# Performance work log

Measured on AMD Instinct MI355X. Metric: run time of the kernel, lower is better.

The kernel has to match this reference:

```python
import jax, jax.numpy as jnp
import numpy as np

NEG = -1e9  # stand-in for -inf mask fill (avoids NaN, softmax weight ~0)
EPS = 1e-5  # torch LayerNorm default


def layer_norm(x, g, b):
    mu = jnp.mean(x, axis=-1, keepdims=True)
    var = jnp.mean(jnp.square(x - mu), axis=-1, keepdims=True)
    return (x - mu) * jax.lax.rsqrt(var + EPS) * g + b


def _forward(x, context, batch_lengths, max_len,
             Wq1, Wk1, Wv1, Wq2, Wk2, Wv2,
             ln1_g, ln1_b, ln2_g, ln2_b, ln3_g, ln3_b,
             fc1_w, fc1_b, fc2_w, fc2_b):
    B, L, E = x.shape
    H, _, dk = Wq1.shape
    pos = jnp.arange(L)
    valid = pos[None, :] < batch_lengths[:, None]                  # [B,L]
    out_mask = valid[:, :, None].astype(x.dtype)                   # [B,L,1] (outputMask)
    key_bias = jnp.where(valid, 0.0, NEG)[:, None, None, :]        # [B,1,1,L] (attnMask on keys)
    causal_bias = jnp.where(pos[:, None] >= pos[None, :], 0.0, NEG)  # [L,L] decoding mask
    scale = 1.0 / jnp.sqrt(jnp.asarray(dk, x.dtype))

    def mha(qk_src, v_src, Wq, Wk, Wv, causal):
        # Q,K from qk_src, V from v_src (faithful to Head.forward)
        m = out_mask[:, None]                                      # [B,1,L,1]
        Q = jnp.einsum('ble,hed->bhld', qk_src, Wq) * m
        K = jnp.einsum('ble,hed->bhld', qk_src, Wk) * m
        V = jnp.einsum('ble,hed->bhld', v_src, Wv) * m
        e = jnp.einsum('bhid,bhjd->bhij', Q, K) + key_bias
        if causal:
            e = e + causal_bias
        s = jax.nn.softmax(e * scale, axis=-1)
        o = jnp.einsum('bhij,bhjd->bhid', s, V)
        return o.transpose(0, 2, 1, 3).reshape(B, L, E)            # concat heads

    z = mha(x, x, Wq1, Wk1, Wv1, causal=True) * out_mask
    x1 = layer_norm(x + z, ln1_g, ln1_b)
    # cross block: Q,K from context, V from x1 (as in source)
    z = mha(context, x1, Wq2, Wk2, Wv2, causal=False) * out_mask
    x2 = layer_norm(x1 + z, ln2_g, ln2_b)
    h = jax.nn.relu(x2 @ fc1_w + fc1_b) * out_mask
    z = (h @ fc2_w + fc2_b) * out_mask
    return layer_norm(x2 + z, ln3_g, ln3_b)


def setup_inputs() -> dict:
    B, L, E, H = 8, 1024, 1024, 16
    dk = E // H
    key = jax.random.key(0)
    ks = jax.random.split(key, 16)
    w = lambda k, s: jax.random.normal(k, s, jnp.float32) * 0.02
    return {
        'x': jax.random.normal(ks[0], (B, L, E), jnp.float32),
        'context': jax.random.normal(ks[1], (B, L, E), jnp.float32),
        'batch_lengths': jax.random.randint(ks[2], (B,), 1, L + 1),
        'max_len': L,
        'Wq1': w(ks[3], (H, E, dk)), 'Wk1': w(ks[4], (H, E, dk)), 'Wv1': w(ks[5], (H, E, dk)),
        'Wq2': w(ks[6], (H, E, dk)), 'Wk2': w(ks[7], (H, E, dk)), 'Wv2': w(ks[8], (H, E, dk)),
        'ln1_g': jnp.ones((E,), jnp.float32), 'ln1_b': jnp.zeros((E,), jnp.float32),
        'ln2_g': jnp.ones((E,), jnp.float32), 'ln2_b': jnp.zeros((E,), jnp.float32),
        'ln3_g': jnp.ones((E,), jnp.float32), 'ln3_b': jnp.zeros((E,), jnp.float32),
        'fc1_w': w(ks[9], (E, E)), 'fc1_b': jnp.zeros((E,), jnp.float32),
        'fc2_w': w(ks[10], (E, E)), 'fc2_b': jnp.zeros((E,), jnp.float32),
    }


def reference(x, context, batch_lengths, max_len,
              Wq1, Wk1, Wv1, Wq2, Wk2, Wv2,
              ln1_g, ln1_b, ln2_g, ln2_b, ln3_g, ln3_b,
              fc1_w, fc1_b, fc2_w, fc2_b):
    return _forward(x, context, batch_lengths, max_len,
                    Wq1, Wk1, Wv1, Wq2, Wk2, Wv2,
                    ln1_g, ln1_b, ln2_g, ln2_b, ln3_g, ln3_b,
                    fc1_w, fc1_b, fc2_w, fc2_b)
```

## Files before the change

### kernel.cpp

```cpp
#include <hip/hip_runtime.h>


typedef unsigned short u16;
typedef unsigned int u32;
typedef __attribute__((ext_vector_type(8))) short bf16x8;
typedef __attribute__((ext_vector_type(4))) float f32x4;

#define Bv 8
#define Lv 1024
#define Ev 1024
#define Hv 16
#define DKv 64
#define Mv (Bv * Lv)

#if defined(__has_builtin)
# if __has_builtin(__builtin_amdgcn_global_load_lds)
#  define HAS_GLL 1
# endif
#endif
#ifndef HAS_GLL
# define HAS_GLL 0
#endif

#if HAS_GLL
__device__ __forceinline__ void gll16(const u16* g, u16* l) {
    __builtin_amdgcn_global_load_lds(
        (const __attribute__((address_space(1))) void*)(unsigned long long)(g),
        (__attribute__((address_space(3))) void*)(unsigned)(unsigned long long)(l),
        16, 0, 0);
}
#endif

__device__ __forceinline__ u16 f2bf(float f) {
    u32 u = __float_as_uint(f);
    u += 0x7fffu + ((u >> 16) & 1u);
    return (u16)(u >> 16);
}
__device__ __forceinline__ u32 pack2(float a, float b) {
    u32 ua = __float_as_uint(a); ua += 0x7fffu + ((ua >> 16) & 1u);
    u32 ub = __float_as_uint(b); ub += 0x7fffu + ((ub >> 16) & 1u);
    return (ua >> 16) | (ub & 0xffff0000u);
}
__device__ __forceinline__ float bf_lo(u32 u) { return __uint_as_float(u << 16); }
__device__ __forceinline__ float bf_hi(u32 u) { return __uint_as_float(u & 0xffff0000u); }

__global__ __launch_bounds__(256) void prep_k(
    const float* __restrict__ x, const float* __restrict__ ctx,
    const float* __restrict__ wq1, const float* __restrict__ wk1, const float* __restrict__ wv1,
    const float* __restrict__ wq2, const float* __restrict__ wk2, const float* __restrict__ wv2,
    const float* __restrict__ f1, const float* __restrict__ f2,
    u16* __restrict__ xb, u16* __restrict__ cb, u16* __restrict__ WT) {
    const int id = blockIdx.x, t = threadIdx.x;
    if (id < 16384) {
        const float* s = (id < 8192) ? x : ctx;
        u16* d = (id < 8192) ? xb : cb;
        const int i4 = ((id & 8191) * 256 + t) * 4;
        float4 v = *(const float4*)(s + i4);
        uint2 o = {pack2(v.x, v.y), pack2(v.z, v.w)};
        *(uint2*)(d + i4) = o;
        return;
    }
    __shared__ float tl[32][33];
    const int tx = t & 31, ty = t >> 5;
    if (id < 16384 + 6144) {
        const int wi = (id - 16384) >> 10;
        const int tile = (id - 16384) & 1023;
        const float* s = (wi == 0) ? wq1 : (wi == 1) ? wk1 : (wi == 2) ? wv1
                       : (wi == 3) ? wq2 : (wi == 4) ? wk2 : wv2;
        u16* d = WT + (size_t)wi * Ev * Ev;
        const int h = tile >> 6, rem = tile & 63;
        const int d0 = (rem & 1) * 32, e0 = (rem >> 1) * 32;
#pragma unroll
        for (int i = 0; i < 4; i++)
            tl[ty + i * 8][tx] = s[(size_t)h * Ev * DKv + (size_t)(e0 + ty + i * 8) * DKv + d0 + tx];
        __syncthreads();
#pragma unroll
        for (int i = 0; i < 4; i++)
            d[(size_t)(h * DKv + d0 + ty + i * 8) * Ev + e0 + tx] = f2bf(tl[tx][ty + i * 8]);
    } else {
        const int wi = (id - 16384 - 6144) >> 10;
        const int tile = (id - 16384 - 6144) & 1023;
        const float* s = wi ? f2 : f1;
        u16* d = WT + (size_t)(6 + wi) * Ev * Ev;
        const int n0 = (tile & 31) * 32, k0 = (tile >> 5) * 32;
#pragma unroll
        for (int i = 0; i < 4; i++)
            tl[ty + i * 8][tx] = s[(size_t)(k0 + ty + i * 8) * Ev + n0 + tx];
        __syncthreads();
#pragma unroll
        for (int i = 0; i < 4; i++)
            d[(size_t)(n0 + ty + i * 8) * Ev + k0 + tx] = f2bf(tl[tx][ty + i * 8]);
    }
}

template <int BIAS, int RELU, int TRANSW>
__global__ __launch_bounds__(256) void mgemm(const u16* __restrict__ A,
                                             const u16* __restrict__ Wt,
                                             const float* __restrict__ bias,
                                             u16* __restrict__ O0, u16* __restrict__ O1,
                                             u16* __restrict__ O2,
                                             const int* __restrict__ lens) {
    __shared__ u16 Alds[2][16 * 512];
    __shared__ u16 Blds[2][16 * 512];
    const int tid = threadIdx.x;
    const int w = tid >> 6, l = tid & 63;
    const int lc = l & 15, lq = l >> 4;
    const int row0 = blockIdx.y * 128, col0 = blockIdx.x * 128;
    const int which = col0 >> 10, colL = col0 & 1023;
    u16* C = (which == 0) ? O0 : (which == 1 ? O1 : O2);
    const bool tr = (TRANSW == which);

    int len = lens[row0 >> 10];
    len = min(max(len, 0), Lv);
    if ((row0 & (Lv - 1)) >= len) {
        const int rr = tid >> 1, cc = (tid & 1) * 64;
        u16* p = tr ? C + (size_t)(colL + rr) * Mv + row0 + cc
                    : C + (size_t)(row0 + rr) * Ev + colL + cc;
        uint4 z4 = {0u, 0u, 0u, 0u};
#pragma unroll
        for (int i = 0; i < 8; i++) *(uint4*)(p + i * 8) = z4;
        return;
    }

    const int wm4 = (w >> 1) * 4, wn4 = (w & 1) * 4;
    f32x4 acc[4][4];
#pragma unroll
    for (int i = 0; i < 4; i++)
#pragma unroll
        for (int j = 0; j < 4; j++) acc[i][j] = (f32x4){0.f, 0.f, 0.f, 0.f};

    const u16* Ag[4]; const u16* Bg[4];
    int lof[4];
#pragma unroll
    for (int i = 0; i < 4; i++) {
        const int g16 = 2 * w + (i >> 1), k32 = i & 1;
        Ag[i] = A  + (size_t)(row0 + g16 * 16 + lc) * Ev + k32 * 32 + lq * 8;
        Bg[i] = Wt + (size_t)(col0 + g16 * 16 + lc) * Ev + k32 * 32 + lq * 8;
        lof[i] = (g16 * 2 + k32) * 512;
    }

#if HAS_GLL
#pragma unroll
    for (int i = 0; i < 4; i++) { gll16(Ag[i], &Alds[0][lof[i]]); gll16(Bg[i], &Blds[0][lof[i]]); }
#else
#pragma unroll
    for (int i = 0; i < 4; i++) {
        *(uint4*)(&Alds[0][lof[i] + l * 8]) = *(const uint4*)Ag[i];
        *(uint4*)(&Blds[0][lof[i] + l * 8]) = *(const uint4*)Bg[i];
    }
#endif
    __syncthreads();

    int cur = 0;
    for (int k0 = 0; k0 < Ev; k0 += 64) {
        if (k0 + 64 < Ev) {
            const int koff = k0 + 64;
#if HAS_GLL
#pragma unroll
            for (int i = 0; i < 4; i++) {
                gll16(Ag[i] + koff, &Alds[cur ^ 1][lof[i]]);
                gll16(Bg[i] + koff, &Blds[cur ^ 1][lof[i]]);
            }
#else
#pragma unroll
            for (int i = 0; i < 4; i++) {
                *(uint4*)(&Alds[cur ^ 1][lof[i] + l * 8]) = *(const uint4*)(Ag[i] + koff);
                *(uint4*)(&Blds[cur ^ 1][lof[i] + l * 8]) = *(const uint4*)(Bg[i] + koff);
            }
#endif
        }
        const u16* Ab = &Alds[cur][0];
        const u16* Bb = &Blds[cur][0];
#pragma unroll
        for (int km = 0; km < 2; km++) {
            bf16x8 af[4], bfr[4];
#pragma unroll
            for (int mt = 0; mt < 4; mt++)
                af[mt] = *(const bf16x8*)(Ab + ((wm4 + mt) * 2 + km) * 512 + l * 8);
#pragma unroll
            for (int nt = 0; nt < 4; nt++)
                bfr[nt] = *(const bf16x8*)(Bb + ((wn4 + nt) * 2 + km) * 512 + l * 8);
#pragma unroll
            for (int mt = 0; mt < 4; mt++)
#pragma unroll
                for (int nt = 0; nt < 4; nt++)
                    acc[mt][nt] = __builtin_amdgcn_mfma_f32_16x16x32_bf16(
                        af[mt], bfr[nt], acc[mt][nt], 0, 0, 0);
        }
        __syncthreads();
        cur ^= 1;
    }

    float bv[4];
#pragma unroll
    for (int nt = 0; nt < 4; nt++)
        bv[nt] = BIAS ? bias[colL + wn4 * 16 + nt * 16 + lc] : 0.f;

#pragma unroll
    for (int mt = 0; mt < 4; mt++) {
        const int rowb = row0 + wm4 * 16 + mt * 16 + lq * 4;
#pragma unroll
        for (int nt = 0; nt < 4; nt++) {
            const int col = colL + wn4 * 16 + nt * 16 + lc;
            float v[4];
#pragma unroll
            for (int r = 0; r < 4; r++) {
                float xv = acc[mt][nt][r] + bv[nt];
                if (RELU) xv = fmaxf(xv, 0.f);
                v[r] = (((rowb + r) & (Lv - 1)) >= len) ? 0.f : xv;
            }
            if (tr) {
                uint2 o = {pack2(v[0], v[1]), pack2(v[2], v[3])};
                *(uint2*)(C + (size_t)col * Mv + rowb) = o;
            } else {
#pragma unroll
                for (int r = 0; r < 4; r++)
                    C[(size_t)(rowb + r) * Ev + col] = f2bf(v[r]);
            }
        }
    }
}

template <int CAUSAL>
__global__ __launch_bounds__(256) void mattn(u16* __restrict__ QZ,
                                             const u16* __restrict__ K,
                                             const u16* __restrict__ VT,
                                             const int* __restrict__ lens) {
    __shared__ u16 Kt[2][16 * 512];
    __shared__ u16 Vt[2][16 * 512];
    __shared__ u16 Pt[4 * 4 * 512];
    const int b = blockIdx.z, h = blockIdx.y, qb = blockIdx.x;
    const int q0 = qb * 128;
    const int tid = threadIdx.x;
    const int w = tid >> 6, l = tid & 63;
    const int lc = l & 15, lq = l >> 4;
    int len = lens[b];
    len = min(max(len, 0), Lv);

    if (q0 >= len) {
        const int zr = tid >> 1, zc = (tid & 1) * 32;
        uint4 z4 = {0u, 0u, 0u, 0u};
        uint4* p = (uint4*)(QZ + (size_t)(b * Lv + q0 + zr) * Ev + h * DKv + zc);
        p[0] = z4; p[1] = z4; p[2] = z4; p[3] = z4;
        return;
    }

    bf16x8 qf[2][2];
#pragma unroll
    for (int mt = 0; mt < 2; mt++)
#pragma unroll
        for (int k2 = 0; k2 < 2; k2++)
            qf[mt][k2] = *(const bf16x8*)(QZ + (size_t)(b * Lv + q0 + w * 32 + mt * 16 + lc) * Ev +
                                          h * DKv + k2 * 32 + lq * 8);

    f32x4 of[2][4];
#pragma unroll
    for (int mt = 0; mt < 2; mt++)
#pragma unroll
        for (int nd = 0; nd < 4; nd++) of[mt][nd] = (f32x4){0.f, 0.f, 0.f, 0.f};
    float mrow[2][4], lrow[2][4];
#pragma unroll
    for (int mt = 0; mt < 2; mt++)
#pragma unroll
        for (int r = 0; r < 4; r++) { mrow[mt][r] = -1e30f; lrow[mt][r] = 0.f; }

    const u16* Kg[4]; const u16* Vg[4];
    int kof[4], vof[4];
#pragma unroll
    for (int i = 0; i < 4; i++) {
        const int k16 = 2 * w + (i >> 1), d32 = i & 1;
        Kg[i] = K + (size_t)(b * Lv + k16 * 16 + lc) * Ev + h * DKv + d32 * 32 + lq * 8;
        kof[i] = (k16 * 2 + d32) * 512;
        Vg[i] = VT + (size_t)(h * DKv + w * 16 + lc) * Mv + b * Lv + i * 32 + lq * 8;
        vof[i] = (w * 4 + i) * 512;
    }
    u16* Pw = Pt + w * 2048;

    const int jend = CAUSAL ? min(len, q0 + 128) : len;
    const int ntiles = (jend + 127) >> 7;

#if HAS_GLL
#pragma unroll
    for (int i = 0; i < 4; i++) {
        gll16(Kg[i], &Kt[0][kof[i]]);
        gll16(Vg[i], &Vt[0][vof[i]]);
    }
#else
#pragma unroll
    for (int i = 0; i < 4; i++) {
        *(uint4*)(&Kt[0][kof[i] + l * 8]) = *(const uint4*)Kg[i];
        *(uint4*)(&Vt[0][vof[i] + l * 8]) = *(const uint4*)Vg[i];
    }
#endif
    __syncthreads();

    int cur = 0;
    for (int kt = 0; kt < ntiles; kt++) {
        const int koff = kt * 128;
        if (kt + 1 < ntiles) {
            const int knext = koff + 128;
#if HAS_GLL
#pragma unroll
            for (int i = 0; i < 4; i++) {
                gll16(Kg[i] + (size_t)knext * Ev, &Kt[cur ^ 1][kof[i]]);
                gll16(Vg[i] + knext, &Vt[cur ^ 1][vof[i]]);
            }
#else
#pragma unroll
            for (int i = 0; i < 4; i++) {
                *(uint4*)(&Kt[cur ^ 1][kof[i] + l * 8]) = *(const uint4*)(Kg[i] + (size_t)knext * Ev);
                *(uint4*)(&Vt[cur ^ 1][vof[i] + l * 8]) = *(const uint4*)(Vg[i] + knext);
            }
#endif
        }
        const u16* Kb = &Kt[cur][0];
        const u16* Vb = &Vt[cur][0];

        f32x4 sf[2][8];
#pragma unroll
        for (int nt = 0; nt < 8; nt++) {
            bf16x8 kf0 = *(const bf16x8*)(Kb + (nt * 2 + 0) * 512 + l * 8);
            bf16x8 kf1 = *(const bf16x8*)(Kb + (nt * 2 + 1) * 512 + l * 8);
#pragma unroll
            for (int mt = 0; mt < 2; mt++) {
                f32x4 s = (f32x4){0.f, 0.f, 0.f, 0.f};
                s = __builtin_amdgcn_mfma_f32_16x16x32_bf16(qf[mt][0], kf0, s, 0, 0, 0);
                s = __builtin_amdgcn_mfma_f32_16x16x32_bf16(qf[mt][1], kf1, s, 0, 0, 0);
                sf[mt][nt] = s;
            }
        }

        float alpha[2][4];
#pragma unroll
        for (int mt = 0; mt < 2; mt++) {
            float tmax[4] = {-1e30f, -1e30f, -1e30f, -1e30f};
#pragma unroll
            for (int nt = 0; nt < 8; nt++) {
                const int jj = koff + nt * 16 + lc;
                const bool jv = jj < len;
#pragma unroll
                for (int r = 0; r < 4; r++) {
                    const int iq = q0 + w * 32 + mt * 16 + lq * 4 + r;
                    const bool valid = jv && (!CAUSAL || jj <= iq);
                    float e = valid ? sf[mt][nt][r] * 0.125f : -1e30f;
                    sf[mt][nt][r] = e;
                    tmax[r] = fmaxf(tmax[r], e);
                }
            }
#pragma unroll
            for (int r = 0; r < 4; r++) {
#pragma unroll
                for (int d = 1; d < 16; d <<= 1)
                    tmax[r] = fmaxf(tmax[r], __shfl_xor(tmax[r], d, 64));
            }
            float psum[4];
#pragma unroll
            for (int r = 0; r < 4; r++) {
                const float mn = fmaxf(mrow[mt][r], tmax[r]);
                alpha[mt][r] = __expf(mrow[mt][r] - mn);
                mrow[mt][r] = mn;
                psum[r] = 0.f;
            }
#pragma unroll
            for (int nt = 0; nt < 8; nt++)
#pragma unroll
                for (int r = 0; r < 4; r++) {
                    float p = __expf(sf[mt][nt][r] - mrow[mt][r]);
                    sf[mt][nt][r] = p;
                    psum[r] += p;
                }
#pragma unroll
            for (int r = 0; r < 4; r++) {
#pragma unroll
                for (int d = 1; d < 16; d <<= 1) psum[r] += __shfl_xor(psum[r], d, 64);
                lrow[mt][r] = lrow[mt][r] * alpha[mt][r] + psum[r];
            }
#pragma unroll
            for (int nd = 0; nd < 4; nd++)
#pragma unroll
                for (int r = 0; r < 4; r++) of[mt][nd][r] *= alpha[mt][r];
        }

#pragma unroll
        for (int mt = 0; mt < 2; mt++) {
#pragma unroll
            for (int nt = 0; nt < 8; nt++)
#pragma unroll
                for (int r = 0; r < 4; r++)
                    Pw[(nt >> 1) * 512 +
                       ((2 * (nt & 1) + (lc >> 3)) * 16 + lq * 4 + r) * 8 + (lc & 7)] =
                        f2bf(sf[mt][nt][r]);
#pragma unroll
            for (int km = 0; km < 4; km++) {
                bf16x8 pa = *(const bf16x8*)(Pw + km * 512 + l * 8);
#pragma unroll
                for (int nd = 0; nd < 4; nd++) {
                    bf16x8 vb = *(const bf16x8*)(Vb + (nd * 4 + km) * 512 + l * 8);
                    of[mt][nd] = __builtin_amdgcn_mfma_f32_16x16x32_bf16(pa, vb, of[mt][nd], 0, 0, 0);
                }
            }
        }
        __syncthreads();
        cur ^= 1;
    }

#pragma unroll
    for (int mt = 0; mt < 2; mt++) {
        float inv[4];
#pragma unroll
        for (int r = 0; r < 4; r++) {
            const int iq = q0 + w * 32 + mt * 16 + lq * 4 + r;
            inv[r] = (iq < len && lrow[mt][r] > 0.f) ? (1.f / lrow[mt][r]) : 0.f;
        }
#pragma unroll
        for (int nd = 0; nd < 4; nd++)
#pragma unroll
            for (int r = 0; r < 4; r++)
                QZ[(size_t)(b * Lv + q0 + w * 32 + mt * 16 + lq * 4 + r) * Ev +
                   h * DKv + nd * 16 + lc] = f2bf(of[mt][nd][r] * inv[r]);
    }
}

template <int BASEBF, int OUTF32>
__global__ __launch_bounds__(256) void ln_k(const void* __restrict__ base,
                                            const u16* __restrict__ z,
                                            const float* __restrict__ g,
                                            const float* __restrict__ bta,
                                            void* __restrict__ out) {
    __shared__ float w1[4], w2[4];
    const int row = blockIdx.x, t = threadIdx.x;
    const int w = t >> 6, l = t & 63;
    const int c0 = t * 4;
    float v[4];
    if (BASEBF) {
        uint2 bu = *(const uint2*)((const u16*)base + (size_t)row * Ev + c0);
        v[0] = bf_lo(bu.x); v[1] = bf_hi(bu.x); v[2] = bf_lo(bu.y); v[3] = bf_hi(bu.y);
    } else {
        float4 f = *(const float4*)((const float*)base + (size_t)row * Ev + c0);
        v[0] = f.x; v[1] = f.y; v[2] = f.z; v[3] = f.w;
    }
    uint2 zu = *(const uint2*)(z + (size_t)row * Ev + c0);
    v[0] += bf_lo(zu.x); v[1] += bf_hi(zu.x); v[2] += bf_lo(zu.y); v[3] += bf_hi(zu.y);
    float s1 = v[0] + v[1] + v[2] + v[3];
    float s2 = v[0] * v[0] + v[1] * v[1] + v[2] * v[2] + v[3] * v[3];
#pragma unroll
    for (int d = 1; d < 64; d <<= 1) {
        s1 += __shfl_xor(s1, d, 64);
        s2 += __shfl_xor(s2, d, 64);
    }
    if (l == 0) { w1[w] = s1; w2[w] = s2; }
    __syncthreads();
    s1 = w1[0] + w1[1] + w1[2] + w1[3];
    s2 = w2[0] + w2[1] + w2[2] + w2[3];
    const float mu = s1 * (1.f / Ev);
    const float var = s2 * (1.f / Ev) - mu * mu;
    const float rinv = rsqrtf(fmaxf(var, 0.f) + 1e-5f);
    float4 gv = *(const float4*)(g + c0);
    float4 bv = *(const float4*)(bta + c0);
    float y[4];
    y[0] = (v[0] - mu) * rinv * gv.x + bv.x;
    y[1] = (v[1] - mu) * rinv * gv.y + bv.y;
    y[2] = (v[2] - mu) * rinv * gv.z + bv.z;
    y[3] = (v[3] - mu) * rinv * gv.w + bv.w;
    if (OUTF32) {
        float4 ow = {y[0], y[1], y[2], y[3]};
        *(float4*)((float*)out + (size_t)row * Ev + c0) = ow;
    } else {
        uint2 ow = {pack2(y[0], y[1]), pack2(y[2], y[3])};
        *(uint2*)((u16*)out + (size_t)row * Ev + c0) = ow;
    }
}

extern "C" void kernel_launch(void* const* d_in, const int* in_sizes, int n_in,
                              void* d_out, int out_size, void* d_ws, size_t ws_size,
                              hipStream_t stream) {
    const float* x    = (const float*)d_in[0];
    const float* ctx  = (const float*)d_in[1];
    const int*   lens = (const int*)d_in[2];
    const float* Wq1 = (const float*)d_in[4];
    const float* Wk1 = (const float*)d_in[5];
    const float* Wv1 = (const float*)d_in[6];
    const float* Wq2 = (const float*)d_in[7];
    const float* Wk2 = (const float*)d_in[8];
    const float* Wv2 = (const float*)d_in[9];
    const float* g1 = (const float*)d_in[10], *b1 = (const float*)d_in[11];
    const float* g2 = (const float*)d_in[12], *b2 = (const float*)d_in[13];
    const float* g3 = (const float*)d_in[14], *b3 = (const float*)d_in[15];
    const float* fc1w = (const float*)d_in[16], *fc1b = (const float*)d_in[17];
    const float* fc2w = (const float*)d_in[18], *fc2b = (const float*)d_in[19];

    const size_t WSZ = (size_t)Ev * Ev;
    const size_t MM  = (size_t)Mv * Ev;
    u16* WT = (u16*)d_ws;
    u16* Wtq1 = WT + 0 * WSZ;
    u16* Wtq2 = WT + 3 * WSZ, *Wtv2 = WT + 5 * WSZ;
    u16* Wtf1 = WT + 6 * WSZ, *Wtf2 = WT + 7 * WSZ;
    u16* B1 = WT + 8 * WSZ;
    u16* B2 = B1 + MM;
    u16* B3 = B2 + MM;
    u16* B4 = B3 + MM;
    u16* xb = (u16*)d_out;
    u16* cb = xb + MM;

    dim3 gP(24576), gQKV(24, 64), gQK(16, 64), gG1(8, 64), gA(8, Hv, Bv), gL(Mv);

    prep_k<<<gP, 256, 0, stream>>>(x, ctx, Wq1, Wk1, Wv1, Wq2, Wk2, Wv2, fc1w, fc2w,
                                   xb, cb, WT);

    mgemm<0, 0, 2><<<gQKV, 256, 0, stream>>>(xb, Wtq1, nullptr, B1, B2, B3, lens);
    mattn<1><<<gA, 256, 0, stream>>>(B1, B2, B3, lens);
    ln_k<0, 0><<<gL, 256, 0, stream>>>(x, B1, g1, b1, B2);

    mgemm<0, 0, -1><<<gQK, 256, 0, stream>>>(cb, Wtq2, nullptr, B1, B3, nullptr, lens);
    mgemm<0, 0, 0><<<gG1, 256, 0, stream>>>(B2, Wtv2, nullptr, B4, nullptr, nullptr, lens);
    mattn<0><<<gA, 256, 0, stream>>>(B1, B3, B4, lens);
    ln_k<1, 0><<<gL, 256, 0, stream>>>(B2, B1, g2, b2, B3);

    mgemm<1, 1, -1><<<gG1, 256, 0, stream>>>(B3, Wtf1, fc1b, B1, nullptr, nullptr, lens);
    mgemm<1, 0, -1><<<gG1, 256, 0, stream>>>(B1, Wtf2, fc2b, B2, nullptr, nullptr, lens);
    ln_k<1, 1><<<gL, 256, 0, stream>>>(B3, B2, g3, b3, d_out);
}
```

Measured before the change: 533.7 us.

## Replace full syncthreads with explicit vmcnt waits and barriers in GEMM and attention pipelines

The GEMM main loop now prefetches two K-tiles ahead into the double buffer. Each step waits with s_waitcnt vmcnt(8) plus s_barrier instead of __syncthreads, so the next tile's global-to-LDS loads stay in flight during compute. The attention loop uses the same partial waitcnt-and-barrier pattern. This is meant to cut the full memory drain at every iteration, at the cost of relying on correct vmcnt counting; a wrong count could cause LDS read/write races. The non-GLL fallback is rewritten to a simpler single-buffer path.

```diff
diff --git a/kernel.cpp b/kernel.cpp
--- a/kernel.cpp
+++ b/kernel.cpp
@@ -142,35 +142,16 @@
 #if HAS_GLL
 #pragma unroll
     for (int i = 0; i < 4; i++) { gll16(Ag[i], &Alds[0][lof[i]]); gll16(Bg[i], &Blds[0][lof[i]]); }
-#else
-#pragma unroll
-    for (int i = 0; i < 4; i++) {
-        *(uint4*)(&Alds[0][lof[i] + l * 8]) = *(const uint4*)Ag[i];
-        *(uint4*)(&Blds[0][lof[i] + l * 8]) = *(const uint4*)Bg[i];
-    }
-#endif
-    __syncthreads();
-
-    int cur = 0;
-    for (int k0 = 0; k0 < Ev; k0 += 64) {
-        if (k0 + 64 < Ev) {
-            const int koff = k0 + 64;
-#if HAS_GLL
-#pragma unroll
-            for (int i = 0; i < 4; i++) {
-                gll16(Ag[i] + koff, &Alds[cur ^ 1][lof[i]]);
-                gll16(Bg[i] + koff, &Blds[cur ^ 1][lof[i]]);
-            }
-#else
-#pragma unroll
-            for (int i = 0; i < 4; i++) {
-                *(uint4*)(&Alds[cur ^ 1][lof[i] + l * 8]) = *(const uint4*)(Ag[i] + koff);
-                *(uint4*)(&Blds[cur ^ 1][lof[i] + l * 8]) = *(const uint4*)(Bg[i] + koff);
-            }
-#endif
-        }
-        const u16* Ab = &Alds[cur][0];
-        const u16* Bb = &Blds[cur][0];
+#pragma unroll
+    for (int i = 0; i < 4; i++) { gll16(Ag[i] + 64, &Alds[1][lof[i]]); gll16(Bg[i] + 64, &Blds[1][lof[i]]); }
+
+    for (int t = 0; t < 16; ++t) {
+        const int p = t & 1;
+        if (t < 15) asm volatile("s_waitcnt vmcnt(8)" ::: "memory");
+        else        asm volatile("s_waitcnt vmcnt(0)" ::: "memory");
+        __builtin_amdgcn_s_barrier();
+        const u16* Ab = &Alds[p][0];
+        const u16* Bb = &Blds[p][0];
 #pragma unroll
         for (int km = 0; km < 2; km++) {
             bf16x8 af[4], bfr[4];
@@ -187,9 +168,44 @@
                     acc[mt][nt] = __builtin_amdgcn_mfma_f32_16x16x32_bf16(
                         af[mt], bfr[nt], acc[mt][nt], 0, 0, 0);
         }
+        __builtin_amdgcn_s_barrier();
+        if (t < 14) {
+            const int koff = (t + 2) * 64;
+#pragma unroll
+            for (int i = 0; i < 4; i++) {
+                gll16(Ag[i] + koff, &Alds[p][lof[i]]);
+                gll16(Bg[i] + koff, &Blds[p][lof[i]]);
+            }
+        }
+    }
+#else
+    for (int t = 0; t < 16; ++t) {
+        const int koff = t * 64;
+#pragma unroll
+        for (int i = 0; i < 4; i++) {
+            *(uint4*)(&Alds[0][lof[i] + l * 8]) = *(const uint4*)(Ag[i] + koff);
+            *(uint4*)(&Blds[0][lof[i] + l * 8]) = *(const uint4*)(Bg[i] + koff);
+        }
         __syncthreads();
-        cur ^= 1;
-    }
+#pragma unroll
+        for (int km = 0; km < 2; km++) {
+            bf16x8 af[4], bfr[4];
+#pragma unroll
+            for (int mt = 0; mt < 4; mt++)
+                af[mt] = *(const bf16x8*)(&Alds[0][((wm4 + mt) * 2 + km) * 512 + l * 8]);
+#pragma unroll
+            for (int nt = 0; nt < 4; nt++)
+                bfr[nt] = *(const bf16x8*)(&Blds[0][((wn4 + nt) * 2 + km) * 512 + l * 8]);
+#pragma unroll
+            for (int mt = 0; mt < 4; mt++)
+#pragma unroll
+                for (int nt = 0; nt < 4; nt++)
+                    acc[mt][nt] = __builtin_amdgcn_mfma_f32_16x16x32_bf16(
+                        af[mt], bfr[nt], acc[mt][nt], 0, 0, 0);
+        }
+        __syncthreads();
+    }
+#endif
 
     float bv[4];
 #pragma unroll
@@ -285,36 +301,45 @@
         gll16(Kg[i], &Kt[0][kof[i]]);
         gll16(Vg[i], &Vt[0][vof[i]]);
     }
-#else
+#endif
+#if !HAS_GLL
 #pragma unroll
     for (int i = 0; i < 4; i++) {
         *(uint4*)(&Kt[0][kof[i] + l * 8]) = *(const uint4*)Kg[i];
         *(uint4*)(&Vt[0][vof[i] + l * 8]) = *(const uint4*)Vg[i];
     }
-#endif
     __syncthreads();
-
-    int cur = 0;
+#endif
+
     for (int kt = 0; kt < ntiles; kt++) {
+        const int p = kt & 1;
         const int koff = kt * 128;
+#if HAS_GLL
         if (kt + 1 < ntiles) {
             const int knext = koff + 128;
-#if HAS_GLL
 #pragma unroll
             for (int i = 0; i < 4; i++) {
-                gll16(Kg[i] + (size_t)knext * Ev, &Kt[cur ^ 1][kof[i]]);
-                gll16(Vg[i] + knext, &Vt[cur ^ 1][vof[i]]);
-            }
+                gll16(Kg[i] + (size_t)knext * Ev, &Kt[p ^ 1][kof[i]]);
+                gll16(Vg[i] + knext, &Vt[p ^ 1][vof[i]]);
+            }
+            asm volatile("s_waitcnt vmcnt(8)" ::: "memory");
+        } else {
+            asm volatile("s_waitcnt vmcnt(0)" ::: "memory");
+        }
+        __builtin_amdgcn_s_barrier();
 #else
+        if (kt > 0) {
+            const int kprev = koff;
 #pragma unroll
             for (int i = 0; i < 4; i++) {
-                *(uint4*)(&Kt[cur ^ 1][kof[i] + l * 8]) = *(const uint4*)(Kg[i] + (size_t)knext * Ev);
-                *(uint4*)(&Vt[cur ^ 1][vof[i] + l * 8]) = *(const uint4*)(Vg[i] + knext);
-            }
-#endif
-        }
-        const u16* Kb = &Kt[cur][0];
-        const u16* Vb = &Vt[cur][0];
+                *(uint4*)(&Kt[p][kof[i] + l * 8]) = *(const uint4*)(Kg[i] + (size_t)kprev * Ev);
+                *(uint4*)(&Vt[p][vof[i] + l * 8]) = *(const uint4*)(Vg[i] + kprev);
+            }
+            __syncthreads();
+        }
+#endif
+        const u16* Kb = &Kt[p][0];
+        const u16* Vb = &Vt[p][0];
 
         f32x4 sf[2][8];
 #pragma unroll
@@ -365,9 +390,9 @@
             for (int nt = 0; nt < 8; nt++)
 #pragma unroll
                 for (int r = 0; r < 4; r++) {
-                    float p = __expf(sf[mt][nt][r] - mrow[mt][r]);
-                    sf[mt][nt][r] = p;
-                    psum[r] += p;
+                    float p2 = __expf(sf[mt][nt][r] - mrow[mt][r]);
+                    sf[mt][nt][r] = p2;
+                    psum[r] += p2;
                 }
 #pragma unroll
             for (int r = 0; r < 4; r++) {
@@ -400,8 +425,11 @@
                 }
             }
         }
+#if HAS_GLL
+        __builtin_amdgcn_s_barrier();
+#else
         __syncthreads();
-        cur ^= 1;
+#endif
     }
 
 #pragma unroll
```

New measurement: 524.9 us. About the same (-1.7%).
